# Optimization experiments

Measured on AMD Instinct MI355X. Metric: run time of the kernel, lower is better.

The kernel has to match this reference:

```python
import jax, jax.numpy as jnp
import numpy as np
import math

NUM_HEADS = 16
HEAD_SIZE = 64
QKT_MEAN = 0.0
QKT_STD = 0.05
APPLY_NOISE = True
NOISE_KEY = jax.random.key(42)


def quantize_activation_8bit(x):
    max_abs = jnp.maximum(jnp.max(jnp.abs(x)), 1e-08)
    scale = max_abs / 127.0
    return jnp.clip(jnp.round(x / scale), -127, 127) * scale


def quantize_weight_4bit(w):
    max_abs = jnp.maximum(jnp.max(jnp.abs(w)), 1e-08)
    scale = max_abs / 7.0
    return jnp.clip(jnp.round(w / scale), -7, 7) * scale


def setup_inputs() -> dict:
    key = jax.random.key(0)
    k1, k2, k3, k4 = jax.random.split(key, 4)
    B, S, D = 4, 1024, 1024
    hidden_states = jax.random.normal(k1, (B, S, D), dtype=jnp.float32)
    attention_mask = jnp.zeros((B, 1, 1, S), dtype=jnp.float32)
    # nn.Linear weights are [out_features, in_features]
    w_scale = 1.0 / math.sqrt(D)
    Wq = jax.random.normal(k2, (D, D), dtype=jnp.float32) * w_scale
    Wk = jax.random.normal(k3, (D, D), dtype=jnp.float32) * w_scale
    Wv = jax.random.normal(k4, (D, D), dtype=jnp.float32) * w_scale
    return {"hidden_states": hidden_states, "attention_mask": attention_mask,
            "Wq": Wq, "Wk": Wk, "Wv": Wv}


def _split_heads(x):
    B, S, _ = x.shape
    return x.reshape(B, S, NUM_HEADS, HEAD_SIZE).transpose(0, 2, 1, 3)  # [B,H,S,Dh]


def reference(hidden_states, attention_mask, Wq, Wk, Wv):
    h_q = quantize_activation_8bit(hidden_states)
    h_k = quantize_activation_8bit(hidden_states)
    Q = _split_heads(jnp.einsum('bsd,od->bso', h_q, quantize_weight_4bit(Wq)))
    K = _split_heads(jnp.einsum('bsd,od->bso', h_k, quantize_weight_4bit(Wk)))
    V = _split_heads(jnp.einsum('bsd,od->bso', hidden_states, quantize_weight_4bit(Wv)))
    qkt = jnp.einsum('bhqd,bhkd->bhqk', Q, K) / math.sqrt(HEAD_SIZE)
    if APPLY_NOISE and QKT_STD > 0:
        noise = jax.random.normal(NOISE_KEY, qkt.shape, dtype=qkt.dtype) * QKT_STD + QKT_MEAN
        qkt = qkt + noise
    qkt = qkt + attention_mask  # [B,1,1,S] broadcasts over [B,H,S,S]
    attn_weights = jax.nn.softmax(qkt, axis=-1)  # dropout is identity in eval
    ctx = jnp.einsum('bhqk,bhkd->bhqd', attn_weights, V)
    B, H, S, Dh = ctx.shape
    ctx = ctx.transpose(0, 2, 1, 3).reshape(B, S, H * Dh)
    return ctx
```

## Files before the change

kernel.cpp:

```cpp
#include <hip/hip_runtime.h>
#include <hip/hip_bf16.h>

typedef unsigned short u16;
typedef unsigned int u32;
typedef __bf16 bf16x8 __attribute__((ext_vector_type(8)));
typedef __bf16 bf16x4 __attribute__((ext_vector_type(4)));
typedef float f32x4 __attribute__((ext_vector_type(4)));

#define MFMA16(a, b, c) __builtin_amdgcn_mfma_f32_16x16x32_bf16((a), (b), (c), 0, 0, 0)

static __device__ __forceinline__ u32 f2bfbits(float f) {
    union { float f; u32 u; } c; c.f = f;
    return (c.u + 0x7FFFu + ((c.u >> 16) & 1u)) >> 16;
}
static __device__ __forceinline__ u32 f2bfbits_exact(float f) {
    union { float f; u32 u; } c; c.f = f;
    return c.u >> 16;
}
static __device__ __forceinline__ u32 pack_bf16x2(float lo, float hi) {
    float2 v; v.x = lo; v.y = hi;
    union { __hip_bfloat162 h; u32 u; } c;
    c.h = __float22bfloat162_rn(v);
    return c.u;
}

static __device__ __forceinline__ u32 rotl_ab(u32 x, int r) {
    return __builtin_amdgcn_alignbit(x, x, 32 - r);
}

static __device__ __forceinline__ float exp2_fast(float x) {
    float r;
    asm("v_exp_f32 %0, %1\n\ts_nop 1" : "=v"(r) : "v"(x));
    return r;
}

static __device__ __forceinline__ void noise_pu8(u32 tk, float* __restrict__ pu) {
    const u32 K1 = 42u, K2 = 0x1BD11BF0u;
    u32 x0[8], x1[8];
#pragma unroll
    for (int d = 0; d < 8; d++) {
        u32 a = tk + (u32)(d < 4 ? d : 12 + d);
        x0[d] = a;
        x1[d] = rotl_ab(a, 13) ^ a;
    }
#define TFR(R)                                             \
    _Pragma("unroll") for (int d = 0; d < 8; d++) {        \
        x0[d] += x1[d];                                    \
        x1[d] = rotl_ab(x1[d], R) ^ x0[d];                 \
    }
#define TFRI(R, A, B)                                      \
    _Pragma("unroll") for (int d = 0; d < 8; d++) {        \
        x1[d] += (B);                                      \
        x0[d] += (A) + x1[d];              \
        x1[d] = rotl_ab(x1[d], R) ^ x0[d];                 \
    }
    TFR(15) TFR(26) TFR(6)
    TFRI(17, K1, K2 + 1u) TFR(29) TFR(16) TFR(24)
    TFRI(13, K2, 2u)      TFR(15) TFR(26) TFR(6)
    TFRI(17, 0u, K1 + 3u) TFR(29) TFR(16) TFR(24)
    TFRI(13, K1, K2 + 4u) TFR(15) TFR(26) TFR(6)
#undef TFR
#undef TFRI
#pragma unroll
    for (int d = 0; d < 8; d++) {
        u32 bits = (x0[d] + K2) ^ (x1[d] + 5u);
        float v2 = __uint_as_float((bits >> 9) | 0x40000000u);
        float u = v2 - 3.0f;
        float t = fmaf(-u, u, 1.0f);
        float L2 = __log2f(t);
        L2 = fmaxf(L2, -7.2134752f);
        float z = fmaf(L2, -0.69314718f, -2.5f);
        float p = 2.81022636e-08f;
        p = fmaf(p, z, 3.43273939e-07f);
        p = fmaf(p, z, -3.5233877e-06f);
        p = fmaf(p, z, -4.39150654e-06f);
        p = fmaf(p, z, 0.00021858087f);
        p = fmaf(p, z, -0.00125372503f);
        p = fmaf(p, z, -0.00417768164f);
        p = fmaf(p, z, 0.246640727f);
        p = fmaf(p, z, 1.50140941f);
        pu[d] = p * u;
    }
}

__global__ __launch_bounds__(256) void absmax_k(const float* __restrict__ h,
                                                const float* __restrict__ wq,
                                                const float* __restrict__ wk,
                                                const float* __restrict__ wv,
                                                u32* __restrict__ slots) {
    int t = blockIdx.y;
    const float* src = (t == 0) ? h : (t == 1) ? wq : (t == 2) ? wk : wv;
    int n4 = ((t == 0) ? 4096 * 1024 : 1024 * 1024) / 4;
    u32 mx = 0;
    int tid = threadIdx.x;
    for (int i = blockIdx.x * blockDim.x + tid; i < n4; i += gridDim.x * blockDim.x) {
        uint4 v = ((const uint4*)src)[i];
        mx = max(mx, v.x & 0x7FFFFFFFu);
        mx = max(mx, v.y & 0x7FFFFFFFu);
        mx = max(mx, v.z & 0x7FFFFFFFu);
        mx = max(mx, v.w & 0x7FFFFFFFu);
    }
    __shared__ u32 red[256];
    red[tid] = mx;
    __syncthreads();
    for (int s = 128; s > 0; s >>= 1) {
        if (tid < s) red[tid] = max(red[tid], red[tid + s]);
        __syncthreads();
    }
    if (tid == 0) atomicMax(&slots[t], red[0]);
}

__global__ __launch_bounds__(256) void prequant_all(const float* __restrict__ hidden,
                                                    const float* __restrict__ wq,
                                                    const float* __restrict__ wk,
                                                    const float* __restrict__ wv,
                                                    u16* __restrict__ hq,
                                                    u16* __restrict__ hbf,
                                                    u16* __restrict__ wqi,
                                                    u16* __restrict__ wki,
                                                    u16* __restrict__ wvi,
                                                    const u32* __restrict__ slots) {
    int y = blockIdx.y;
    const float* src = (y == 0) ? hidden : (y == 1) ? wq : (y == 2) ? wk : wv;
    u16* dqi = (y == 0) ? hq : (y == 1) ? wqi : (y == 2) ? wki : wvi;
    u16* draw = (y == 0) ? hbf : nullptr;
    float qmax = (y == 0) ? 127.0f : 7.0f;
    int n8 = ((y == 0) ? 4096 * 1024 : 1024 * 1024) / 8;

    float amax = fmaxf(__uint_as_float(slots[y]), 1e-8f);
    float scale = amax / qmax;
    for (int i = blockIdx.x * blockDim.x + threadIdx.x; i < n8; i += gridDim.x * blockDim.x) {
        float4 a = ((const float4*)src)[2 * i];
        float4 b = ((const float4*)src)[2 * i + 1];
        float x[8] = {a.x, a.y, a.z, a.w, b.x, b.y, b.z, b.w};
        u16 qi[8], rw[8];
#pragma unroll
        for (int j = 0; j < 8; j++) {
            float q = fminf(fmaxf(rintf(x[j] / scale), -qmax), qmax);
            qi[j] = (u16)f2bfbits_exact(q);
            rw[j] = (u16)f2bfbits(x[j]);
        }
        *(uint4*)(dqi + 8 * (size_t)i) = *(const uint4*)qi;
        if (draw) *(uint4*)(draw + 8 * (size_t)i) = *(const uint4*)rw;
    }
}

__global__ __launch_bounds__(256, 2) void qkv_gemm_all(const u16* __restrict__ hq,
                                                       const u16* __restrict__ hbf,
                                                       const u16* __restrict__ wqi,
                                                       const u16* __restrict__ wki,
                                                       const u16* __restrict__ wvi,
                                                       const u32* __restrict__ slots,
                                                       u16* __restrict__ Qb,
                                                       u16* __restrict__ Kb,
                                                       u16* __restrict__ Vtb) {
    __shared__ __align__(16) u16 As[128 * 40];
    __shared__ __align__(16) u16 Bs[128 * 40];
    int z = blockIdx.z;
    const u16* A  = (z < 2) ? hq : hbf;
    const u16* Bw = (z == 0) ? wqi : (z == 1) ? wki : wvi;
    u16* outp     = (z == 0) ? Qb : (z == 1) ? Kb : Vtb;
    int transOut = (z == 2);
    float s_a = fmaxf(__uint_as_float(slots[0]), 1e-8f) / 127.0f;
    float s_w = fmaxf(__uint_as_float(slots[z + 1]), 1e-8f) / 7.0f;
    float oscale = (z < 2) ? (s_a * s_w) : s_w;

    int tid = threadIdx.x;
    int srow = tid >> 2, scol = (tid & 3) * 8;
    int mbase = blockIdx.x * 128, nbase = blockIdx.y * 128;
    int lane = tid & 63, w = tid >> 6;
    int wv_m = w & 1, wv_n = w >> 1;
    int quad = lane >> 4, l16 = lane & 15;

    f32x4 acc[4][4];
#pragma unroll
    for (int i = 0; i < 4; i++)
#pragma unroll
        for (int j = 0; j < 4; j++) acc[i][j] = (f32x4){0.f, 0.f, 0.f, 0.f};

    const u16* aptr0 = A + (size_t)(mbase + srow) * 1024 + scol;
    const u16* aptr1 = A + (size_t)(mbase + 64 + srow) * 1024 + scol;
    const u16* bptr0 = Bw + (size_t)(nbase + srow) * 1024 + scol;
    const u16* bptr1 = Bw + (size_t)(nbase + 64 + srow) * 1024 + scol;

    for (int k0 = 0; k0 < 1024; k0 += 32) {
        uint4 a0 = *(const uint4*)(aptr0 + k0);
        uint4 a1 = *(const uint4*)(aptr1 + k0);
        uint4 b0 = *(const uint4*)(bptr0 + k0);
        uint4 b1 = *(const uint4*)(bptr1 + k0);
        __syncthreads();
        *(uint4*)(As + srow * 40 + scol) = a0;
        *(uint4*)(As + (64 + srow) * 40 + scol) = a1;
        *(uint4*)(Bs + srow * 40 + scol) = b0;
        *(uint4*)(Bs + (64 + srow) * 40 + scol) = b1;
        __syncthreads();
        bf16x8 af[4], bfr[4];
#pragma unroll
        for (int mt = 0; mt < 4; mt++)
            af[mt] = *(const bf16x8*)(As + (wv_m * 64 + mt * 16 + l16) * 40 + quad * 8);
#pragma unroll
        for (int nt = 0; nt < 4; nt++)
            bfr[nt] = *(const bf16x8*)(Bs + (wv_n * 64 + nt * 16 + l16) * 40 + quad * 8);
#pragma unroll
        for (int mt = 0; mt < 4; mt++)
#pragma unroll
            for (int nt = 0; nt < 4; nt++)
                acc[mt][nt] = MFMA16(af[mt], bfr[nt], acc[mt][nt]);
    }

#pragma unroll
    for (int mt = 0; mt < 4; mt++)
#pragma unroll
        for (int nt = 0; nt < 4; nt++)
#pragma unroll
            for (int r = 0; r < 4; r++) {
                float val = acc[mt][nt][r] * oscale;
                int m = mbase + wv_m * 64 + mt * 16 + quad * 4 + r;
                int o = nbase + wv_n * 64 + nt * 16 + l16;
                int b = m >> 10, s = m & 1023;
                int hh = o >> 6, dh = o & 63;
                size_t off = transOut ? (((size_t)(b * 16 + hh) * 64 + dh) * 1024 + s)
                                      : (((size_t)(b * 16 + hh) * 1024 + s) * 64 + dh);
                outp[off] = (u16)f2bfbits(val);
            }
}

__global__ __launch_bounds__(256, 4) void attn_kernel(const u16* __restrict__ Q,
                                                      const u16* __restrict__ K,
                                                      const u16* __restrict__ Vt,
                                                      const float* __restrict__ mask,
                                                      float* __restrict__ O0,
                                                      float* __restrict__ O1,
                                                      float* __restrict__ l0,
                                                      float* __restrict__ l1) {
    __shared__ float msk[512];
    int qt = blockIdx.x, h = blockIdx.y;
    int b = blockIdx.z & 3, split = blockIdx.z >> 2;
    int bh = b * 16 + h;
    int tid = threadIdx.x, wv = tid >> 6, lane = tid & 63;
    int quad = lane >> 4, l16 = lane & 15;
    int q0 = qt * 64 + wv * 16;
    int ks0 = split * 512;

    const float IL2 = 1.4426950408889634f;
    const float* maskb = mask + b * 1024 + ks0;
    msk[tid] = maskb[tid] * IL2;
    msk[tid + 256] = maskb[tid + 256] * IL2;
    __syncthreads();

    float* Obuf = split ? O1 : O0;
    float* lbuf = split ? l1 : l0;
    const u16* Qb = Q + (size_t)bh * 1024 * 64;
    const u16* Kb = K + (size_t)bh * 1024 * 64;
    const u16* Vb = Vt + (size_t)bh * 64 * 1024 + ks0;

    bf16x8 aq0 = *(const bf16x8*)(Qb + (q0 + l16) * 64 + quad * 8);
    bf16x8 aq1 = *(const bf16x8*)(Qb + (q0 + l16) * 64 + 32 + quad * 8);

    f32x4 oacc[4];
#pragma unroll
    for (int i = 0; i < 4; i++) oacc[i] = (f32x4){0.f, 0.f, 0.f, 0.f};
    float lsum = 0.f;

    u32 tbase = ((u32)(bh * 1024 + q0 + l16)) * 1024u + (u32)ks0 + (u32)(4 * quad) + 42u;

    const float C_S = 0.18033688011112042f;
    const float C_N = 0.10201394645f;

    for (int kk = 0; kk < 512; kk += 32) {
        const u16* Kt = Kb + (size_t)(ks0 + kk) * 64;
        bf16x8 bk0 = *(const bf16x8*)(Kt + l16 * 64 + quad * 8);
        bf16x8 bk1 = *(const bf16x8*)(Kt + l16 * 64 + 32 + quad * 8);
        bf16x8 bk2 = *(const bf16x8*)(Kt + (16 + l16) * 64 + quad * 8);
        bf16x8 bk3 = *(const bf16x8*)(Kt + (16 + l16) * 64 + 32 + quad * 8);

        const u16* Vk = Vb + kk + 4 * quad;
        bf16x4 vlo[4], vhi[4];
#pragma unroll
        for (int nt = 0; nt < 4; nt++) {
            vlo[nt] = *(const bf16x4*)(Vk + (nt * 16 + l16) * 1024);
            vhi[nt] = *(const bf16x4*)(Vk + (nt * 16 + l16) * 1024 + 16);
        }

        int mb = kk + 4 * quad;
        float mk[4], mh[4];
#pragma unroll
        for (int r = 0; r < 4; r++) { mk[r] = msk[mb + r]; mh[r] = msk[mb + 16 + r]; }

        float pu[8];
        noise_pu8(tbase + (u32)kk, pu);

        f32x4 s0 = (f32x4){0.f, 0.f, 0.f, 0.f};
        f32x4 s1 = (f32x4){0.f, 0.f, 0.f, 0.f};
        s0 = MFMA16(bk0, aq0, s0);
        s0 = MFMA16(bk1, aq1, s0);
        s1 = MFMA16(bk2, aq0, s1);
        s1 = MFMA16(bk3, aq1, s1);

        float e[8];
#pragma unroll
        for (int r = 0; r < 4; r++) {
            e[r]     = exp2_fast(fmaf(pu[r],     C_N, fmaf(s0[r], C_S, mk[r])));
            e[4 + r] = exp2_fast(fmaf(pu[4 + r], C_N, fmaf(s1[r], C_S, mh[r])));
        }
        lsum += ((e[0] + e[1]) + (e[2] + e[3])) + ((e[4] + e[5]) + (e[6] + e[7]));

        union { u32 u[4]; bf16x8 v; } pf;
        pf.u[0] = pack_bf16x2(e[0], e[1]);
        pf.u[1] = pack_bf16x2(e[2], e[3]);
        pf.u[2] = pack_bf16x2(e[4], e[5]);
        pf.u[3] = pack_bf16x2(e[6], e[7]);

#pragma unroll
        for (int nt = 0; nt < 4; nt++) {
            bf16x8 vf = __builtin_shufflevector(vlo[nt], vhi[nt], 0, 1, 2, 3, 4, 5, 6, 7);
            oacc[nt] = MFMA16(pf.v, vf, oacc[nt]);
        }
    }

    float l = lsum;
    l += __shfl_xor(l, 16);
    l += __shfl_xor(l, 32);
    if (lane < 16) lbuf[bh * 1024 + q0 + lane] = l;
#pragma unroll
    for (int nt = 0; nt < 4; nt++) {
#pragma unroll
        for (int r = 0; r < 4; r++) {
            int q = q0 + quad * 4 + r;
            int dh = nt * 16 + l16;
            Obuf[((size_t)(b * 1024 + q)) * 1024 + h * 64 + dh] = oacc[nt][r];
        }
    }
}

__global__ __launch_bounds__(256) void combine_k(float* __restrict__ outp,
                                                 const float* __restrict__ O1,
                                                 const float* __restrict__ l0,
                                                 const float* __restrict__ l1) {
    int gid = blockIdx.x * 256 + threadIdx.x;
    int e = gid << 2;
    int bq = e >> 10;
    int h = (e & 1023) >> 6;
    int b = bq >> 10, q = bq & 1023;
    int lidx = ((b * 16 + h) << 10) + q;
    float linv = 1.0f / (l0[lidx] + l1[lidx]);
    float4 a = ((const float4*)outp)[gid];
    float4 c = ((const float4*)O1)[gid];
    float4 o;
    o.x = (a.x + c.x) * linv;
    o.y = (a.y + c.y) * linv;
    o.z = (a.z + c.z) * linv;
    o.w = (a.w + c.w) * linv;
    ((float4*)outp)[gid] = o;
}

extern "C" void kernel_launch(void* const* d_in, const int* in_sizes, int n_in,
                              void* d_out, int out_size, void* d_ws, size_t ws_size,
                              hipStream_t stream) {
    (void)in_sizes; (void)n_in; (void)out_size; (void)ws_size;
    const float* hidden = (const float*)d_in[0];
    const float* maskp  = (const float*)d_in[1];
    const float* Wq     = (const float*)d_in[2];
    const float* Wk     = (const float*)d_in[3];
    const float* Wv     = (const float*)d_in[4];
    float* outp = (float*)d_out;

    char* ws = (char*)d_ws;
    u32* slots = (u32*)ws;
    u16* hq  = (u16*)(ws + 256);
    u16* hbf = hq + 4096 * 1024;
    u16* wqi = hbf + 4096 * 1024;
    u16* wki = wqi + 1024 * 1024;
    u16* wvi = wki + 1024 * 1024;
    u16* Qb  = wvi + 1024 * 1024;
    u16* Kb  = Qb + 4096 * 1024;
    u16* Vtb = Kb + 4096 * 1024;

    float* O1buf = (float*)hq;
    float* l0buf = (float*)wqi;
    float* l1buf = l0buf + 4 * 16 * 1024;

    hipMemsetAsync(slots, 0, 16, stream);
    absmax_k<<<dim3(128, 4), 256, 0, stream>>>(hidden, Wq, Wk, Wv, slots);
    prequant_all<<<dim3(64, 4), 256, 0, stream>>>(hidden, Wq, Wk, Wv,
                                                  hq, hbf, wqi, wki, wvi, slots);
    qkv_gemm_all<<<dim3(32, 8, 3), 256, 0, stream>>>(hq, hbf, wqi, wki, wvi, slots,
                                                     Qb, Kb, Vtb);
    attn_kernel<<<dim3(16, 16, 8), 256, 0, stream>>>(Qb, Kb, Vtb, maskp,
                                                     outp, O1buf, l0buf, l1buf);
    combine_k<<<dim3(4096), 256, 0, stream>>>(outp, O1buf, l0buf, l1buf);
}
```

Measured before the change: 343.2 us.

## Double-buffer K/V tiles in registers and compute row sums via MFMA

The attention inner loop now prefetches the next 32-key K/V tile into a second register set while the current tile is processed, so global load latency overlaps with the MFMA and exp work. The softmax denominator is no longer built from scalar adds and shuffles; it accumulates with an extra MFMA against a ones vector, and the mask is read as vectorized f32x4 from aligned LDS. The extra registers for the second tile come with a lower launch-bounds occupancy hint (3 instead of 4), which may reduce latency hiding across waves. Row sums are now taken from bf16-rounded probabilities, matching the values fed to the PV product.

```diff
diff --git a/kernel.cpp b/kernel.cpp
--- a/kernel.cpp
+++ b/kernel.cpp
@@ -225,7 +225,70 @@
             }
 }
 
-__global__ __launch_bounds__(256, 4) void attn_kernel(const u16* __restrict__ Q,
+struct KVTile {
+    bf16x8 bk0, bk1, bk2, bk3;
+    bf16x4 vlo[4], vhi[4];
+};
+
+static __device__ __forceinline__ void load_tile(KVTile& t,
+                                                 const u16* __restrict__ Kb,
+                                                 const u16* __restrict__ Vb,
+                                                 int ks0, int kk, int l16, int quad) {
+    const u16* Kt = Kb + (size_t)(ks0 + kk) * 64;
+    t.bk0 = *(const bf16x8*)(Kt + l16 * 64 + quad * 8);
+    t.bk1 = *(const bf16x8*)(Kt + l16 * 64 + 32 + quad * 8);
+    t.bk2 = *(const bf16x8*)(Kt + (16 + l16) * 64 + quad * 8);
+    t.bk3 = *(const bf16x8*)(Kt + (16 + l16) * 64 + 32 + quad * 8);
+    const u16* Vk = Vb + kk + 4 * quad;
+#pragma unroll
+    for (int nt = 0; nt < 4; nt++) {
+        t.vlo[nt] = *(const bf16x4*)(Vk + (nt * 16 + l16) * 1024);
+        t.vhi[nt] = *(const bf16x4*)(Vk + (nt * 16 + l16) * 1024 + 16);
+    }
+}
+
+static __device__ __forceinline__ void phase(const KVTile& t,
+                                             f32x4 (&oacc)[4], f32x4& lacc,
+                                             u32 tk, const float* __restrict__ msk,
+                                             int kk, int quad,
+                                             bf16x8 aq0, bf16x8 aq1, bf16x8 ones) {
+    const float C_S = 0.18033688011112042f;
+    const float C_N = 0.10201394645f;
+
+    f32x4 mk4 = *(const f32x4*)(msk + kk + 4 * quad);
+    f32x4 mh4 = *(const f32x4*)(msk + kk + 16 + 4 * quad);
+
+    float pu[8];
+    noise_pu8(tk, pu);
+
+    f32x4 s0 = (f32x4){0.f, 0.f, 0.f, 0.f};
+    f32x4 s1 = (f32x4){0.f, 0.f, 0.f, 0.f};
+    s0 = MFMA16(t.bk0, aq0, s0);
+    s0 = MFMA16(t.bk1, aq1, s0);
+    s1 = MFMA16(t.bk2, aq0, s1);
+    s1 = MFMA16(t.bk3, aq1, s1);
+
+    float e[8];
+#pragma unroll
+    for (int r = 0; r < 4; r++) {
+        e[r]     = exp2_fast(fmaf(pu[r],     C_N, fmaf(s0[r], C_S, mk4[r])));
+        e[4 + r] = exp2_fast(fmaf(pu[4 + r], C_N, fmaf(s1[r], C_S, mh4[r])));
+    }
+    union { u32 u[4]; bf16x8 v; } pf;
+    pf.u[0] = pack_bf16x2(e[0], e[1]);
+    pf.u[1] = pack_bf16x2(e[2], e[3]);
+    pf.u[2] = pack_bf16x2(e[4], e[5]);
+    pf.u[3] = pack_bf16x2(e[6], e[7]);
+
+#pragma unroll
+    for (int nt = 0; nt < 4; nt++) {
+        bf16x8 vf = __builtin_shufflevector(t.vlo[nt], t.vhi[nt], 0, 1, 2, 3, 4, 5, 6, 7);
+        oacc[nt] = MFMA16(pf.v, vf, oacc[nt]);
+    }
+    lacc = MFMA16(pf.v, ones, lacc);
+}
+
+__global__ __launch_bounds__(256, 3) void attn_kernel(const u16* __restrict__ Q,
                                                       const u16* __restrict__ K,
                                                       const u16* __restrict__ Vt,
                                                       const float* __restrict__ mask,
@@ -233,7 +296,7 @@
                                                       float* __restrict__ O1,
                                                       float* __restrict__ l0,
                                                       float* __restrict__ l1) {
-    __shared__ float msk[512];
+    __shared__ __align__(16) float msk[512];
     int qt = blockIdx.x, h = blockIdx.y;
     int b = blockIdx.z & 3, split = blockIdx.z >> 2;
     int bh = b * 16 + h;
@@ -257,71 +320,33 @@
     bf16x8 aq0 = *(const bf16x8*)(Qb + (q0 + l16) * 64 + quad * 8);
     bf16x8 aq1 = *(const bf16x8*)(Qb + (q0 + l16) * 64 + 32 + quad * 8);
 
+    union { u32 u[4]; bf16x8 v; } ones;
+#pragma unroll
+    for (int i = 0; i < 4; i++) ones.u[i] = 0x3F803F80u;
+
     f32x4 oacc[4];
 #pragma unroll
     for (int i = 0; i < 4; i++) oacc[i] = (f32x4){0.f, 0.f, 0.f, 0.f};
-    float lsum = 0.f;
+    f32x4 lacc = (f32x4){0.f, 0.f, 0.f, 0.f};
 
     u32 tbase = ((u32)(bh * 1024 + q0 + l16)) * 1024u + (u32)ks0 + (u32)(4 * quad) + 42u;
 
-    const float C_S = 0.18033688011112042f;
-    const float C_N = 0.10201394645f;
-
-    for (int kk = 0; kk < 512; kk += 32) {
-        const u16* Kt = Kb + (size_t)(ks0 + kk) * 64;
-        bf16x8 bk0 = *(const bf16x8*)(Kt + l16 * 64 + quad * 8);
-        bf16x8 bk1 = *(const bf16x8*)(Kt + l16 * 64 + 32 + quad * 8);
-        bf16x8 bk2 = *(const bf16x8*)(Kt + (16 + l16) * 64 + quad * 8);
-        bf16x8 bk3 = *(const bf16x8*)(Kt + (16 + l16) * 64 + 32 + quad * 8);
-
-        const u16* Vk = Vb + kk + 4 * quad;
-        bf16x4 vlo[4], vhi[4];
-#pragma unroll
-        for (int nt = 0; nt < 4; nt++) {
-            vlo[nt] = *(const bf16x4*)(Vk + (nt * 16 + l16) * 1024);
-            vhi[nt] = *(const bf16x4*)(Vk + (nt * 16 + l16) * 1024 + 16);
-        }
-
-        int mb = kk + 4 * quad;
-        float mk[4], mh[4];
-#pragma unroll
-        for (int r = 0; r < 4; r++) { mk[r] = msk[mb + r]; mh[r] = msk[mb + 16 + r]; }
-
-        float pu[8];
-        noise_pu8(tbase + (u32)kk, pu);
-
-        f32x4 s0 = (f32x4){0.f, 0.f, 0.f, 0.f};
-        f32x4 s1 = (f32x4){0.f, 0.f, 0.f, 0.f};
-        s0 = MFMA16(bk0, aq0, s0);
-        s0 = MFMA16(bk1, aq1, s0);
-        s1 = MFMA16(bk2, aq0, s1);
-        s1 = MFMA16(bk3, aq1, s1);
-
-        float e[8];
-#pragma unroll
-        for (int r = 0; r < 4; r++) {
-            e[r]     = exp2_fast(fmaf(pu[r],     C_N, fmaf(s0[r], C_S, mk[r])));
-            e[4 + r] = exp2_fast(fmaf(pu[4 + r], C_N, fmaf(s1[r], C_S, mh[r])));
-        }
-        lsum += ((e[0] + e[1]) + (e[2] + e[3])) + ((e[4] + e[5]) + (e[6] + e[7]));
-
-        union { u32 u[4]; bf16x8 v; } pf;
-        pf.u[0] = pack_bf16x2(e[0], e[1]);
-        pf.u[1] = pack_bf16x2(e[2], e[3]);
-        pf.u[2] = pack_bf16x2(e[4], e[5]);
-        pf.u[3] = pack_bf16x2(e[6], e[7]);
-
-#pragma unroll
-        for (int nt = 0; nt < 4; nt++) {
-            bf16x8 vf = __builtin_shufflevector(vlo[nt], vhi[nt], 0, 1, 2, 3, 4, 5, 6, 7);
-            oacc[nt] = MFMA16(pf.v, vf, oacc[nt]);
-        }
-    }
-
-    float l = lsum;
-    l += __shfl_xor(l, 16);
-    l += __shfl_xor(l, 32);
-    if (lane < 16) lbuf[bh * 1024 + q0 + lane] = l;
+    KVTile tA, tB;
+    load_tile(tA, Kb, Vb, ks0, 0, l16, quad);
+
+    for (int kk = 0; kk < 512; kk += 64) {
+        load_tile(tB, Kb, Vb, ks0, kk + 32, l16, quad);
+        phase(tA, oacc, lacc, tbase + (u32)kk, msk, kk, quad, aq0, aq1, ones.v);
+        if (kk + 64 < 512)
+            load_tile(tA, Kb, Vb, ks0, kk + 64, l16, quad);
+        phase(tB, oacc, lacc, tbase + (u32)(kk + 32), msk, kk + 32, quad, aq0, aq1, ones.v);
+    }
+
+    if (l16 == 0) {
+        int lbase = bh * 1024 + q0 + quad * 4;
+#pragma unroll
+        for (int r = 0; r < 4; r++) lbuf[lbase + r] = lacc[r];
+    }
 #pragma unroll
     for (int nt = 0; nt < 4; nt++) {
 #pragma unroll
```

New measurement: 343.2 us. About the same (+0.0%).
